# Kernel tuning notes

Measured on AMD Instinct MI355X. Metric: run time of the kernel, lower is better.

Reference implementation:

```python
import jax, jax.numpy as jnp
import numpy as np

N = 100000
E = 1600000
IN_C, HID_C, OUT_C = 128, 128, 64


def setup_inputs() -> dict:
    key = jax.random.key(0)
    ks = jax.random.split(key, 8)
    x = jax.random.normal(ks[0], (N, IN_C), dtype=jnp.float32)
    edge_index = jax.random.randint(ks[1], (2, E), 0, N, dtype=jnp.int64)

    def glorot(k, fan_in, fan_out):
        s = jnp.sqrt(6.0 / (fan_in + fan_out))
        return jax.random.uniform(k, (fan_in, fan_out), jnp.float32, -s, s)

    W1 = glorot(ks[2], IN_C, HID_C)
    b1 = jnp.zeros((HID_C,), jnp.float32)
    W2 = glorot(ks[3], HID_C, HID_C)
    b2 = jnp.zeros((HID_C,), jnp.float32)
    W3 = glorot(ks[4], HID_C, OUT_C)
    b3 = jnp.zeros((OUT_C,), jnp.float32)
    return {"x": x, "edge_index": edge_index,
            "W1": W1, "b1": b1, "W2": W2, "b2": b2, "W3": W3, "b3": b3}


def _gcn_norm(row, col, n_nodes):
    # symmetric normalization, add_self_loops=False (PyG gcn_norm)
    deg = jax.ops.segment_sum(jnp.ones(row.shape[0], jnp.float32), col, num_segments=n_nodes)
    dinv = jnp.where(deg > 0, jax.lax.rsqrt(jnp.maximum(deg, 1.0)), 0.0)
    dinv = jnp.where(deg > 0, deg ** -0.5, 0.0)
    return dinv[row] * dinv[col]  # [E]


def _gcn_conv(x, row, col, norm, W, b):
    h = x @ W                                # [N, F_out] dense GEMM first (PyG order)
    msg = h[row] * norm[:, None]             # gather + scale, [E, F_out]
    out = jax.ops.segment_sum(msg, col, num_segments=x.shape[0])  # scatter-add
    return out + b


def reference(x, edge_index, W1, b1, W2, b2, W3, b3):
    row, col = edge_index[0], edge_index[1]
    norm = _gcn_norm(row, col, x.shape[0])
    h = jax.nn.relu(_gcn_conv(x, row, col, norm, W1, b1))   # dropout is identity in eval
    h = jax.nn.relu(_gcn_conv(h, row, col, norm, W2, b2))
    out = _gcn_conv(h, row, col, norm, W3, b3)
    return out
```

## Files before the change

kernel.cpp:

```cpp
#include <hip/hip_runtime.h>
#include <hip/hip_bf16.h>
#include <hip/hip_fp16.h>


#define K_DIM 128
#define NSEG 4
#define SEGW 25600

typedef _Float16 f16x8 __attribute__((ext_vector_type(8)));
typedef float f32x4 __attribute__((ext_vector_type(4)));

static inline long long cdiv_ll(long long a, long long b) { return (a + b - 1) / b; }

__global__ __launch_bounds__(256) void count2_kernel(const int* __restrict__ row, const int* __restrict__ col,
                                                     int* __restrict__ cnt2, int* __restrict__ rank2, int E) {
    int e = blockIdx.x * 256 + threadIdx.x;
    if (e < E) {
        int key = col[e] * NSEG + row[e] / SEGW;
        rank2[e] = atomicAdd(&cnt2[key], 1);
    }
}

__global__ __launch_bounds__(256) void dinv_kernel(const int* __restrict__ cnt2, float* __restrict__ dinv, int N) {
    int n = blockIdx.x * 256 + threadIdx.x;
    if (n < N) {
        int d = 0;
#pragma unroll
        for (int s = 0; s < NSEG; ++s) d += cnt2[n * NSEG + s];
        dinv[n] = (d > 0) ? (1.0f / sqrtf((float)d)) : 0.0f;
    }
}

__global__ __launch_bounds__(256) void scan1_kernel(int* __restrict__ data, int* __restrict__ bsum, int M) {
    __shared__ int lds[256];
    const int t = threadIdx.x;
    const int base = blockIdx.x * 4096;
    int v[16], s = 0;
#pragma unroll
    for (int j = 0; j < 16; ++j) {
        int i = base + t * 16 + j;
        v[j] = (i < M) ? data[i] : 0;
        s += v[j];
    }
    lds[t] = s;
    __syncthreads();
    for (int d = 1; d < 256; d <<= 1) {
        int x = (t >= d) ? lds[t - d] : 0;
        __syncthreads();
        lds[t] += x;
        __syncthreads();
    }
    int excl = lds[t] - s;
    if (t == 255) bsum[blockIdx.x] = lds[255];
    int run = excl;
#pragma unroll
    for (int j = 0; j < 16; ++j) {
        int i = base + t * 16 + j;
        if (i < M) data[i] = run;
        run += v[j];
    }
}

__global__ __launch_bounds__(256) void scan2_kernel(int* __restrict__ bsum, int G, int* __restrict__ data,
                                                    int M, int E) {
    __shared__ int lds[256];
    const int t = threadIdx.x;
    int s = (t < G) ? bsum[t] : 0;
    lds[t] = s;
    __syncthreads();
    for (int d = 1; d < 256; d <<= 1) {
        int x = (t >= d) ? lds[t - d] : 0;
        __syncthreads();
        lds[t] += x;
        __syncthreads();
    }
    if (t < G) bsum[t] = lds[t] - s;
    if (t == 0) data[M] = E;
}

__global__ __launch_bounds__(256) void scan3_kernel(int* __restrict__ data, const int* __restrict__ bsum, int M) {
    int add = bsum[blockIdx.x];
    const int base = blockIdx.x * 4096;
#pragma unroll
    for (int j = 0; j < 16; ++j) {
        int i = base + threadIdx.x * 16 + j;
        if (i < M) data[i] += add;
    }
}

__global__ __launch_bounds__(256) void fill_kernel(const int* __restrict__ row, const int* __restrict__ col,
                                                   const int* __restrict__ off2, const int* __restrict__ rank2,
                                                   int* __restrict__ csr_row, int E) {
    int e = blockIdx.x * 256 + threadIdx.x;
    if (e < E) {
        int r = row[e];
        int key = col[e] * NSEG + r / SEGW;
        int idx = off2[key] + rank2[e];
        __builtin_nontemporal_store(r, &csr_row[idx]);
    }
}

template <int COUT>
__global__ __launch_bounds__(256) void pack_w_kernel(const float* __restrict__ W, _Float16* __restrict__ Wp) {
    constexpr int NT = COUT / 16;
    int t = blockIdx.x * 256 + threadIdx.x;
    if (t >= 4 * NT * 64) return;
    int lane = t & 63;
    int nt = (t >> 6) % NT;
    int kt = t / (64 * NT);
    int c = lane & 15, q = lane >> 4;
    f16x8 v;
#pragma unroll
    for (int j = 0; j < 8; ++j) {
        int k = kt * 32 + q * 8 + j;
        v[j] = (_Float16)W[k * COUT + nt * 16 + c];
    }
    *(f16x8*)&Wp[(size_t)t * 8] = v;
}

template <int COUT, bool AF16>
__global__ __launch_bounds__(256) void gemm_mfma(const void* __restrict__ Av, const _Float16* __restrict__ Wp,
                                                 const float* __restrict__ dinv, _Float16* __restrict__ Cmat, int M) {
    constexpr int NT = COUT / 16;
    constexpr int NFRAG = 4 * NT * 64;
    __shared__ _Float16 Wlds[NFRAG * 8];

    const int t = threadIdx.x;
    for (int i = t; i < NFRAG; i += 256)
        *(f16x8*)&Wlds[(size_t)i * 8] = *(const f16x8*)&Wp[(size_t)i * 8];
    __syncthreads();

    const int lane = t & 63;
    const int wave = t >> 6;
    const int c = lane & 15;
    const int q = lane >> 4;
    const int row_base = blockIdx.x * 128 + wave * 32;

    f32x4 acc[2][NT];
#pragma unroll
    for (int rt = 0; rt < 2; ++rt)
#pragma unroll
        for (int nt = 0; nt < NT; ++nt) {
            acc[rt][nt][0] = 0.f; acc[rt][nt][1] = 0.f;
            acc[rt][nt][2] = 0.f; acc[rt][nt][3] = 0.f;
        }

#pragma unroll
    for (int kt = 0; kt < 4; ++kt) {
        f16x8 a[2];
#pragma unroll
        for (int rt = 0; rt < 2; ++rt) {
            int r = row_base + rt * 16 + c;
            r = (r < M) ? r : (M - 1);
            if (AF16) {
                const _Float16* Ap = (const _Float16*)Av;
                a[rt] = *(const f16x8*)&Ap[((size_t)kt * M + r) * 32 + q * 8];
            } else {
                const float* ap = (const float*)Av + (size_t)r * K_DIM + kt * 32 + q * 8;
                float4 v0 = *(const float4*)ap;
                float4 v1 = *(const float4*)(ap + 4);
                f16x8 av;
                av[0] = (_Float16)v0.x; av[1] = (_Float16)v0.y;
                av[2] = (_Float16)v0.z; av[3] = (_Float16)v0.w;
                av[4] = (_Float16)v1.x; av[5] = (_Float16)v1.y;
                av[6] = (_Float16)v1.z; av[7] = (_Float16)v1.w;
                a[rt] = av;
            }
        }
#pragma unroll
        for (int nt = 0; nt < NT; ++nt) {
            f16x8 b = *(const f16x8*)&Wlds[(size_t)((kt * NT + nt) * 64 + lane) * 8];
            acc[0][nt] = __builtin_amdgcn_mfma_f32_16x16x32_f16(a[0], b, acc[0][nt], 0, 0, 0);
            acc[1][nt] = __builtin_amdgcn_mfma_f32_16x16x32_f16(a[1], b, acc[1][nt], 0, 0, 0);
        }
    }

#pragma unroll
    for (int rt = 0; rt < 2; ++rt)
#pragma unroll
        for (int reg = 0; reg < 4; ++reg) {
            int row = row_base + rt * 16 + q * 4 + reg;
            if (row < M) {
                float dv = dinv[row];
#pragma unroll
                for (int nt = 0; nt < NT; ++nt)
                    Cmat[((size_t)(nt >> 1) * M + row) * 32 + (nt & 1) * 16 + c] =
                        (_Float16)(acc[rt][nt][reg] * dv);
            }
        }
}

template <int NSP, bool RELU, typename OutT>
__global__ __launch_bounds__(256) void gather_direct(const _Float16* __restrict__ g, const int* __restrict__ off2,
                                                     const int* __restrict__ csr_row, const float* __restrict__ dinv,
                                                     const float* __restrict__ bias, OutT* __restrict__ outp, int N) {
    constexpr int NTILE = 64;
    __shared__ int bounds[NTILE * NSEG + 1];

    const int t = threadIdx.x;
    const int plane = blockIdx.x % NSP;
    const int node0 = (blockIdx.x / NSP) * NTILE;
    const int M4 = N * NSEG;
    const int base = node0 * NSEG;

    for (int i = t; i < NTILE * NSEG + 1; i += 256) {
        int idx = base + i;
        bounds[i] = off2[idx < M4 ? idx : M4];
    }
    __syncthreads();

    const int j = t & 3;
    const int n_loc = t >> 2;
    const int node = node0 + n_loc;
    const _Float16* gp = g + (size_t)plane * N * 32 + j * 8;

    float acc[8];
#pragma unroll
    for (int k = 0; k < 8; ++k) acc[k] = 0.f;

#pragma unroll
    for (int s = 0; s < NSEG; ++s) {
        const int e0 = bounds[n_loc * NSEG + s];
        const int e1 = bounds[n_loc * NSEG + s + 1];
        for (int e = e0; e < e1; ++e) {
            int r = csr_row[e];
            f16x8 v = *(const f16x8*)&gp[(size_t)r * 32];
#pragma unroll
            for (int k = 0; k < 8; ++k) acc[k] += (float)v[k];
        }
    }

    if (node < N) {
        float dv = dinv[node];
        float o[8];
#pragma unroll
        for (int k = 0; k < 8; ++k) {
            o[k] = acc[k] * dv + bias[plane * 32 + j * 8 + k];
            if (RELU) o[k] = fmaxf(o[k], 0.f);
        }
        if constexpr (sizeof(OutT) == 2) {
            f16x8 hv;
#pragma unroll
            for (int k = 0; k < 8; ++k) hv[k] = (_Float16)o[k];
            *(f16x8*)((_Float16*)outp + ((size_t)plane * N + node) * 32 + j * 8) = hv;
        } else {
            float* op = (float*)outp + (size_t)node * 64 + plane * 32 + j * 8;
            *(float4*)op = make_float4(o[0], o[1], o[2], o[3]);
            *(float4*)(op + 4) = make_float4(o[4], o[5], o[6], o[7]);
        }
    }
}

extern "C" void kernel_launch(void* const* d_in, const int* in_sizes, int n_in,
                              void* d_out, int out_size, void* d_ws, size_t ws_size,
                              hipStream_t stream) {
    const float* x  = (const float*)d_in[0];
    const int*   ei = (const int*)d_in[1];
    const float* W1 = (const float*)d_in[2];
    const float* b1 = (const float*)d_in[3];
    const float* W2 = (const float*)d_in[4];
    const float* b2 = (const float*)d_in[5];
    const float* W3 = (const float*)d_in[6];
    const float* b3 = (const float*)d_in[7];

    const int N = in_sizes[0] / 128;
    const int E = in_sizes[1] / 2;
    const int* row = ei;
    const int* col = ei + E;
    const int M4 = N * NSEG;
    const int G = (int)cdiv_ll(M4, 4096);

    char* wsb = (char*)d_ws;
    int*      off2    = (int*)wsb;      wsb += (size_t)(M4 + 1) * 4;
    float*    dinv    = (float*)wsb;    wsb += (size_t)N * 4;
    int*      bsum    = (int*)wsb;      wsb += 256 * 4;
    int*      rank2   = (int*)wsb;      wsb += (size_t)E * 4;
    int*      csr_row = (int*)wsb;      wsb += (size_t)E * 4;
    wsb = (char*)((((uintptr_t)wsb) + 255) & ~(uintptr_t)255);
    _Float16* Wp1     = (_Float16*)wsb; wsb += 16384 * 2;
    _Float16* Wp2     = (_Float16*)wsb; wsb += 16384 * 2;
    _Float16* Wp3     = (_Float16*)wsb; wsb += 8192 * 2;
    _Float16* bufA    = (_Float16*)wsb; wsb += (size_t)N * 128 * 2;
    _Float16* bufB    = (_Float16*)wsb;
    float*    out     = (float*)d_out;

    hipMemsetAsync(off2, 0, (size_t)M4 * 4, stream);
    count2_kernel<<<cdiv_ll(E, 256), 256, 0, stream>>>(row, col, off2, rank2, E);
    dinv_kernel<<<cdiv_ll(N, 256), 256, 0, stream>>>(off2, dinv, N);
    scan1_kernel<<<G, 256, 0, stream>>>(off2, bsum, M4);
    scan2_kernel<<<1, 256, 0, stream>>>(bsum, G, off2, M4, E);
    scan3_kernel<<<G, 256, 0, stream>>>(off2, bsum, M4);
    fill_kernel<<<cdiv_ll(E, 256), 256, 0, stream>>>(row, col, off2, rank2, csr_row, E);
    pack_w_kernel<128><<<8, 256, 0, stream>>>(W1, Wp1);
    pack_w_kernel<128><<<8, 256, 0, stream>>>(W2, Wp2);
    pack_w_kernel<64><<<4, 256, 0, stream>>>(W3, Wp3);

    const long long gemmBlocks = cdiv_ll(N, 128);
    const long long nt64       = cdiv_ll(N, 64);

    gemm_mfma<128, false><<<gemmBlocks, 256, 0, stream>>>(x, Wp1, dinv, bufA, N);
    gather_direct<4, true, _Float16><<<nt64 * 4, 256, 0, stream>>>(bufA, off2, csr_row, dinv, b1, bufB, N);

    gemm_mfma<128, true><<<gemmBlocks, 256, 0, stream>>>(bufB, Wp2, dinv, bufA, N);
    gather_direct<4, true, _Float16><<<nt64 * 4, 256, 0, stream>>>(bufA, off2, csr_row, dinv, b2, bufB, N);

    gemm_mfma<64, true><<<gemmBlocks, 256, 0, stream>>>(bufB, Wp3, dinv, bufA, N);
    gather_direct<2, false, float><<<nt64 * 2, 256, 0, stream>>>(bufA, off2, csr_row, dinv, b3, out, N);
}
```

Baseline: 502.7 us.

## Use 8 source segments and persistent gather blocks covering multiple node tiles

Doubles the number of source-row segments in the CSR ordering (NSEG 8) and replaces the per-tile gather with a fixed grid of 1024 blocks, each accumulating several 64-node tiles. Segments are iterated in the outer loop across all tiles of a block, so concurrent gathers touch a narrower source range, aiming at better L2/cache reuse of the gathered rows. It trades this for more registers per thread, drops the LDS staging of bounds, and hardcodes a grid size that only covers N up to about 114k nodes.

```diff
diff --git a/kernel.cpp b/kernel.cpp
--- a/kernel.cpp
+++ b/kernel.cpp
@@ -4,8 +4,8 @@
 
 
 #define K_DIM 128
-#define NSEG 4
-#define SEGW 25600
+#define NSEG 8
+#define SEGW 12500
 
 typedef _Float16 f16x8 __attribute__((ext_vector_type(8)));
 typedef float f32x4 __attribute__((ext_vector_type(4)));
@@ -190,63 +190,64 @@
         }
 }
 
-template <int NSP, bool RELU, typename OutT>
-__global__ __launch_bounds__(256) void gather_direct(const _Float16* __restrict__ g, const int* __restrict__ off2,
-                                                     const int* __restrict__ csr_row, const float* __restrict__ dinv,
-                                                     const float* __restrict__ bias, OutT* __restrict__ outp, int N) {
-    constexpr int NTILE = 64;
-    __shared__ int bounds[NTILE * NSEG + 1];
-
+template <int NSP, int TPB, bool RELU, typename OutT>
+__global__ __launch_bounds__(256, 4) void gather_persist(const _Float16* __restrict__ g,
+                                                         const int* __restrict__ off2,
+                                                         const int* __restrict__ csr_row,
+                                                         const float* __restrict__ dinv,
+                                                         const float* __restrict__ bias,
+                                                         OutT* __restrict__ outp, int N) {
     const int t = threadIdx.x;
     const int plane = blockIdx.x % NSP;
-    const int node0 = (blockIdx.x / NSP) * NTILE;
-    const int M4 = N * NSEG;
-    const int base = node0 * NSEG;
-
-    for (int i = t; i < NTILE * NSEG + 1; i += 256) {
-        int idx = base + i;
-        bounds[i] = off2[idx < M4 ? idx : M4];
-    }
-    __syncthreads();
-
+    const int slot  = blockIdx.x / NSP;
     const int j = t & 3;
     const int n_loc = t >> 2;
-    const int node = node0 + n_loc;
     const _Float16* gp = g + (size_t)plane * N * 32 + j * 8;
 
-    float acc[8];
-#pragma unroll
-    for (int k = 0; k < 8; ++k) acc[k] = 0.f;
-
-#pragma unroll
+    float acc[TPB][8];
+#pragma unroll
+    for (int r = 0; r < TPB; ++r)
+#pragma unroll
+        for (int k = 0; k < 8; ++k) acc[r][k] = 0.f;
+
     for (int s = 0; s < NSEG; ++s) {
-        const int e0 = bounds[n_loc * NSEG + s];
-        const int e1 = bounds[n_loc * NSEG + s + 1];
-        for (int e = e0; e < e1; ++e) {
-            int r = csr_row[e];
-            f16x8 v = *(const f16x8*)&gp[(size_t)r * 32];
-#pragma unroll
-            for (int k = 0; k < 8; ++k) acc[k] += (float)v[k];
-        }
-    }
-
-    if (node < N) {
-        float dv = dinv[node];
-        float o[8];
-#pragma unroll
-        for (int k = 0; k < 8; ++k) {
-            o[k] = acc[k] * dv + bias[plane * 32 + j * 8 + k];
-            if (RELU) o[k] = fmaxf(o[k], 0.f);
-        }
-        if constexpr (sizeof(OutT) == 2) {
-            f16x8 hv;
-#pragma unroll
-            for (int k = 0; k < 8; ++k) hv[k] = (_Float16)o[k];
-            *(f16x8*)((_Float16*)outp + ((size_t)plane * N + node) * 32 + j * 8) = hv;
-        } else {
-            float* op = (float*)outp + (size_t)node * 64 + plane * 32 + j * 8;
-            *(float4*)op = make_float4(o[0], o[1], o[2], o[3]);
-            *(float4*)(op + 4) = make_float4(o[4], o[5], o[6], o[7]);
+#pragma unroll
+        for (int r = 0; r < TPB; ++r) {
+            int node = (slot * TPB + r) * 64 + n_loc;
+            if (node < N) {
+                int e0 = off2[node * NSEG + s];
+                int e1 = off2[node * NSEG + s + 1];
+                for (int e = e0; e < e1; ++e) {
+                    int src = csr_row[e];
+                    f16x8 v = *(const f16x8*)&gp[(size_t)src * 32];
+#pragma unroll
+                    for (int k = 0; k < 8; ++k) acc[r][k] += (float)v[k];
+                }
+            }
+        }
+    }
+
+#pragma unroll
+    for (int r = 0; r < TPB; ++r) {
+        int node = (slot * TPB + r) * 64 + n_loc;
+        if (node < N) {
+            float dv = dinv[node];
+            float o[8];
+#pragma unroll
+            for (int k = 0; k < 8; ++k) {
+                o[k] = acc[r][k] * dv + bias[plane * 32 + j * 8 + k];
+                if (RELU) o[k] = fmaxf(o[k], 0.f);
+            }
+            if constexpr (sizeof(OutT) == 2) {
+                f16x8 hv;
+#pragma unroll
+                for (int k = 0; k < 8; ++k) hv[k] = (_Float16)o[k];
+                *(f16x8*)((_Float16*)outp + ((size_t)plane * N + node) * 32 + j * 8) = hv;
+            } else {
+                float* op = (float*)outp + (size_t)node * 64 + plane * 32 + j * 8;
+                *(float4*)op = make_float4(o[0], o[1], o[2], o[3]);
+                *(float4*)(op + 4) = make_float4(o[4], o[5], o[6], o[7]);
+            }
         }
     }
 }
@@ -267,11 +268,11 @@
     const int E = in_sizes[1] / 2;
     const int* row = ei;
     const int* col = ei + E;
-    const int M4 = N * NSEG;
-    const int G = (int)cdiv_ll(M4, 4096);
+    const int M8 = N * NSEG;
+    const int G = (int)cdiv_ll(M8, 4096);
 
     char* wsb = (char*)d_ws;
-    int*      off2    = (int*)wsb;      wsb += (size_t)(M4 + 1) * 4;
+    int*      off2    = (int*)wsb;      wsb += (size_t)(M8 + 1) * 4;
     float*    dinv    = (float*)wsb;    wsb += (size_t)N * 4;
     int*      bsum    = (int*)wsb;      wsb += 256 * 4;
     int*      rank2   = (int*)wsb;      wsb += (size_t)E * 4;
@@ -284,26 +285,25 @@
     _Float16* bufB    = (_Float16*)wsb;
     float*    out     = (float*)d_out;
 
-    hipMemsetAsync(off2, 0, (size_t)M4 * 4, stream);
+    hipMemsetAsync(off2, 0, (size_t)M8 * 4, stream);
     count2_kernel<<<cdiv_ll(E, 256), 256, 0, stream>>>(row, col, off2, rank2, E);
     dinv_kernel<<<cdiv_ll(N, 256), 256, 0, stream>>>(off2, dinv, N);
-    scan1_kernel<<<G, 256, 0, stream>>>(off2, bsum, M4);
-    scan2_kernel<<<1, 256, 0, stream>>>(bsum, G, off2, M4, E);
-    scan3_kernel<<<G, 256, 0, stream>>>(off2, bsum, M4);
+    scan1_kernel<<<G, 256, 0, stream>>>(off2, bsum, M8);
+    scan2_kernel<<<1, 256, 0, stream>>>(bsum, G, off2, M8, E);
+    scan3_kernel<<<G, 256, 0, stream>>>(off2, bsum, M8);
     fill_kernel<<<cdiv_ll(E, 256), 256, 0, stream>>>(row, col, off2, rank2, csr_row, E);
     pack_w_kernel<128><<<8, 256, 0, stream>>>(W1, Wp1);
     pack_w_kernel<128><<<8, 256, 0, stream>>>(W2, Wp2);
     pack_w_kernel<64><<<4, 256, 0, stream>>>(W3, Wp3);
 
     const long long gemmBlocks = cdiv_ll(N, 128);
-    const long long nt64       = cdiv_ll(N, 64);
 
     gemm_mfma<128, false><<<gemmBlocks, 256, 0, stream>>>(x, Wp1, dinv, bufA, N);
-    gather_direct<4, true, _Float16><<<nt64 * 4, 256, 0, stream>>>(bufA, off2, csr_row, dinv, b1, bufB, N);
+    gather_persist<4, 7, true, _Float16><<<1024, 256, 0, stream>>>(bufA, off2, csr_row, dinv, b1, bufB, N);
 
     gemm_mfma<128, true><<<gemmBlocks, 256, 0, stream>>>(bufB, Wp2, dinv, bufA, N);
-    gather_direct<4, true, _Float16><<<nt64 * 4, 256, 0, stream>>>(bufA, off2, csr_row, dinv, b2, bufB, N);
+    gather_persist<4, 7, true, _Float16><<<1024, 256, 0, stream>>>(bufA, off2, csr_row, dinv, b2, bufB, N);
 
     gemm_mfma<64, true><<<gemmBlocks, 256, 0, stream>>>(bufB, Wp3, dinv, bufA, N);
-    gather_direct<2, false, float><<<nt64 * 2, 256, 0, stream>>>(bufA, off2, csr_row, dinv, b3, out, N);
-}
+    gather_persist<2, 4, false, float><<<1024, 256, 0, stream>>>(bufA, off2, csr_row, dinv, b3, out, N);
+}
```

Result: slower. 737.1 us (+46.6%).
